# Optimization experiments

Hardware: AMD Instinct MI355X
Metric: run time of the kernel (lower is better)

The kernel has to match this reference:

```python
import math
import jax, jax.numpy as jnp
import numpy as np

DIM = 1024
N_HEADS = 16
N_KV_HEADS = 4
HEAD_DIM = 64
WINDOW = 512
EPS = 1e-6
B, S = 2, 2048

def _alibi_slopes(n_heads):
    def pow2(n):
        r = 2.0 ** (-8.0 / n)
        return np.array([r ** (i + 1) for i in range(n)], dtype=np.float32)
    if math.log2(n_heads).is_integer():
        return pow2(n_heads)
    m = 2 ** math.floor(math.log2(n_heads))
    return np.concatenate([pow2(m), pow2(2 * m)[::2][: n_heads - m]])

def _rmsnorm(x, w, eps=EPS):
    var = jnp.mean(x * x, axis=-1, keepdims=True)
    return x * jax.lax.rsqrt(var + eps) * w

def setup_inputs() -> dict:
    key = jax.random.key(0)
    ks = jax.random.split(key, 8)
    x = jax.random.normal(ks[0], (B, S, DIM), dtype=jnp.float32)
    wq = 0.02 * jax.random.normal(ks[1], (N_HEADS * HEAD_DIM, DIM), dtype=jnp.float32)
    wk = 0.02 * jax.random.normal(ks[2], (N_KV_HEADS * HEAD_DIM, DIM), dtype=jnp.float32)
    wv = 0.02 * jax.random.normal(ks[3], (N_KV_HEADS * HEAD_DIM, DIM), dtype=jnp.float32)
    wo = 0.02 * jax.random.normal(ks[4], (DIM, N_HEADS * HEAD_DIM), dtype=jnp.float32)
    q_norm_w = jnp.ones((N_HEADS * HEAD_DIM,), dtype=jnp.float32)
    k_norm_w = jnp.ones((N_KV_HEADS * HEAD_DIM,), dtype=jnp.float32)
    return {"x": x, "wq": wq, "wk": wk, "wv": wv, "wo": wo,
            "q_norm_w": q_norm_w, "k_norm_w": k_norm_w}

def reference(x, wq, wk, wv, wo, q_norm_w, k_norm_w):
    bsz, seqlen, _ = x.shape
    repeats = N_HEADS // N_KV_HEADS
    xq = _rmsnorm(x @ wq.T, q_norm_w)
    xk = _rmsnorm(x @ wk.T, k_norm_w)
    xv = x @ wv.T
    # [b, h, s, d]
    q = xq.reshape(bsz, seqlen, N_HEADS, HEAD_DIM).transpose(0, 2, 1, 3)
    k = xk.reshape(bsz, seqlen, N_KV_HEADS, HEAD_DIM).transpose(0, 2, 1, 3)
    v = xv.reshape(bsz, seqlen, N_KV_HEADS, HEAD_DIM).transpose(0, 2, 1, 3)
    k = jnp.repeat(k, repeats, axis=1)
    v = jnp.repeat(v, repeats, axis=1)
    pos = jnp.arange(seqlen)
    rel = pos[None, :] - pos[:, None]  # [s_q, s_k], key - query
    slopes = jnp.asarray(_alibi_slopes(N_HEADS))
    bias = slopes[:, None, None] * rel[None].astype(x.dtype)  # [h, s, s]
    masked = (rel > 0) | (rel < -WINDOW)  # causal + sliding window
    bias = jnp.where(masked[None], -jnp.inf, bias)
    scale = 1.0 / math.sqrt(HEAD_DIM)
    scores = jnp.einsum('bhqd,bhkd->bhqk', q, k) * scale + bias[None]
    probs = jax.nn.softmax(scores, axis=-1)
    y = jnp.einsum('bhqk,bhkd->bhqd', probs, v)
    y = y.transpose(0, 2, 1, 3).reshape(bsz, seqlen, N_HEADS * HEAD_DIM)
    return y @ wo.T
```

## Files before the change

kernel.cpp:

```cpp
#include <hip/hip_runtime.h>

typedef unsigned short u16;
typedef unsigned int u32;

typedef __bf16 bf16x8 __attribute__((ext_vector_type(8)));
typedef float f32x4 __attribute__((ext_vector_type(4)));

__device__ __forceinline__ u16 f2bf(float f) {
  u32 u = __builtin_bit_cast(u32, f);
  u32 r = (u + 0x7fffu + ((u >> 16) & 1u)) >> 16;
  return (u16)r;
}
__device__ __forceinline__ float bf2f(u16 v) {
  u32 u = (u32)v << 16;
  return __builtin_bit_cast(float, u);
}

__global__ __launch_bounds__(256)
void cvt_all_kernel(const float* __restrict__ x, const float* __restrict__ wq,
                    const float* __restrict__ wk, const float* __restrict__ wv,
                    const float* __restrict__ wo, u16* __restrict__ x_bf,
                    u16* __restrict__ wcat_bf, u16* __restrict__ wo_bf) {
  int t = blockIdx.x * 256 + threadIdx.x;
  const float* src;
  u16* dst;
  if (t < 1048576) {
    src = x; dst = x_bf;
  } else if (t < 1310720) {
    src = wq; dst = wcat_bf; t -= 1048576;
  } else if (t < 1376256) {
    src = wk; dst = wcat_bf + 1048576; t -= 1310720;
  } else if (t < 1441792) {
    src = wv; dst = wcat_bf + 1310720; t -= 1376256;
  } else {
    src = wo; dst = wo_bf; t -= 1441792;
  }
  const int i = t * 4;
  float4 v = *(const float4*)(src + i);
  uint2 p;
  p.x = (u32)f2bf(v.x) | ((u32)f2bf(v.y) << 16);
  p.y = (u32)f2bf(v.z) | ((u32)f2bf(v.w) << 16);
  *(uint2*)(dst + i) = p;
}

template <typename OutT>
__global__ __launch_bounds__(256)
void gemm_bt_kernel(const u16* __restrict__ A, const u16* __restrict__ B,
                    OutT* __restrict__ C, int M, int N, int K) {
  __shared__ u16 As[64 * 64];
  __shared__ u16 Bs[128 * 64];
  const int tid = threadIdx.x;
  const int lane = tid & 63;
  const int wave = tid >> 6;
  const int wm = (wave >> 1) * 32;
  const int wn = (wave & 1) * 64;
  const int l15 = lane & 15;
  const int quad = lane >> 4;
  const int sw = l15 & 7;
  const size_t bm = (size_t)blockIdx.y * 64;
  const size_t bn = (size_t)blockIdx.x * 128;

  f32x4 acc[2][4];
#pragma unroll
  for (int i = 0; i < 2; ++i)
#pragma unroll
    for (int j = 0; j < 4; ++j) acc[i][j] = f32x4{0.f, 0.f, 0.f, 0.f};

  const int ra0 = tid >> 3, ba0 = tid & 7;
  const int ra1 = (tid + 256) >> 3, ba1 = tid & 7;
  const u16* Ap0 = A + (bm + ra0) * (size_t)K + ba0 * 8;
  const u16* Ap1 = A + (bm + ra1) * (size_t)K + ba1 * 8;
  const u16* Bp0 = B + (bn + ra0) * (size_t)K + ba0 * 8;
  const u16* Bp1 = B + (bn + ra1) * (size_t)K + ba1 * 8;
  const u16* Bp2 = B + (bn + ra0 + 64) * (size_t)K + ba0 * 8;
  const u16* Bp3 = B + (bn + ra1 + 64) * (size_t)K + ba1 * 8;
  const int wa0 = ra0 * 64 + ((ba0 ^ (ra0 & 7)) * 8);
  const int wa1 = ra1 * 64 + ((ba1 ^ (ra1 & 7)) * 8);
  const int wb2 = (ra0 + 64) * 64 + ((ba0 ^ (ra0 & 7)) * 8);
  const int wb3 = (ra1 + 64) * 64 + ((ba1 ^ (ra1 & 7)) * 8);

  uint4 a0 = *(const uint4*)Ap0, a1 = *(const uint4*)Ap1;
  uint4 b0 = *(const uint4*)Bp0, b1 = *(const uint4*)Bp1;
  uint4 b2 = *(const uint4*)Bp2, b3 = *(const uint4*)Bp3;

  for (int k0 = 0; k0 < K; k0 += 64) {
    __syncthreads();
    *(uint4*)(&As[wa0]) = a0;
    *(uint4*)(&As[wa1]) = a1;
    *(uint4*)(&Bs[wa0]) = b0;
    *(uint4*)(&Bs[wa1]) = b1;
    *(uint4*)(&Bs[wb2]) = b2;
    *(uint4*)(&Bs[wb3]) = b3;
    __syncthreads();
    const int kn = (k0 + 64 < K) ? k0 + 64 : 0;
    a0 = *(const uint4*)(Ap0 + kn);
    a1 = *(const uint4*)(Ap1 + kn);
    b0 = *(const uint4*)(Bp0 + kn);
    b1 = *(const uint4*)(Bp1 + kn);
    b2 = *(const uint4*)(Bp2 + kn);
    b3 = *(const uint4*)(Bp3 + kn);
#pragma unroll
    for (int h = 0; h < 2; ++h) {
      const int cb = (quad + 4 * h);
      bf16x8 af[2], bfr[4];
#pragma unroll
      for (int i = 0; i < 2; ++i)
        af[i] = *(const bf16x8*)(&As[(wm + i * 16 + l15) * 64 + ((cb ^ sw) * 8)]);
#pragma unroll
      for (int j = 0; j < 4; ++j)
        bfr[j] = *(const bf16x8*)(&Bs[(wn + j * 16 + l15) * 64 + ((cb ^ sw) * 8)]);
#pragma unroll
      for (int i = 0; i < 2; ++i)
#pragma unroll
        for (int j = 0; j < 4; ++j)
          acc[i][j] = __builtin_amdgcn_mfma_f32_16x16x32_bf16(af[i], bfr[j], acc[i][j], 0, 0, 0);
    }
  }

  const int rq = quad * 4;
#pragma unroll
  for (int i = 0; i < 2; ++i) {
#pragma unroll
    for (int r = 0; r < 4; ++r) {
      OutT* crow = C + (bm + wm + i * 16 + rq + r) * (size_t)N + bn + wn + l15;
#pragma unroll
      for (int j = 0; j < 4; ++j) {
        if constexpr (sizeof(OutT) == 2)
          crow[j * 16] = f2bf(acc[i][j][r]);
        else
          crow[j * 16] = acc[i][j][r];
      }
    }
  }
}

__global__ __launch_bounds__(256)
void norm_vtrans_kernel(u16* __restrict__ qkv, const float* __restrict__ qw,
                        const float* __restrict__ kw, u16* __restrict__ vt) {
  __shared__ u16 shmem[64 * 72];
  const int bid = blockIdx.x;
  const int tid = threadIdx.x;
  if (bid < 4096) {
    float* red = (float*)shmem;
    u16* row = qkv + (size_t)bid * 1536;
    uint2 pk = *(const uint2*)(row + tid * 4);
    float v0 = bf2f((u16)pk.x), v1 = bf2f((u16)(pk.x >> 16));
    float v2 = bf2f((u16)pk.y), v3 = bf2f((u16)(pk.y >> 16));
    float ss = v0 * v0 + v1 * v1 + v2 * v2 + v3 * v3;
#pragma unroll
    for (int off = 32; off > 0; off >>= 1) ss += __shfl_down(ss, off);
    if ((tid & 63) == 0) red[tid >> 6] = ss;
    __syncthreads();
    float tot = red[0] + red[1] + red[2] + red[3];
    float rn = rsqrtf(tot * (1.0f / 1024.0f) + 1e-6f);
    float4 w = *(const float4*)(qw + tid * 4);
    uint2 po;
    po.x = (u32)f2bf(v0 * rn * w.x) | ((u32)f2bf(v1 * rn * w.y) << 16);
    po.y = (u32)f2bf(v2 * rn * w.z) | ((u32)f2bf(v3 * rn * w.w) << 16);
    *(uint2*)(row + tid * 4) = po;
    if (tid < 64) {
      uint2 kp = *(const uint2*)(row + 1024 + tid * 4);
      float k0 = bf2f((u16)kp.x), k1 = bf2f((u16)(kp.x >> 16));
      float k2 = bf2f((u16)kp.y), k3 = bf2f((u16)(kp.y >> 16));
      float sk = k0 * k0 + k1 * k1 + k2 * k2 + k3 * k3;
#pragma unroll
      for (int off = 32; off > 0; off >>= 1) sk += __shfl_down(sk, off);
      float tk = __shfl(sk, 0);
      float rk = rsqrtf(tk * (1.0f / 256.0f) + 1e-6f);
      float4 w2 = *(const float4*)(kw + tid * 4);
      uint2 ko;
      ko.x = (u32)f2bf(k0 * rk * w2.x) | ((u32)f2bf(k1 * rk * w2.y) << 16);
      ko.y = (u32)f2bf(k2 * rk * w2.z) | ((u32)f2bf(k3 * rk * w2.w) << 16);
      *(uint2*)(row + 1024 + tid * 4) = ko;
    }
  } else {
    const int e = bid - 4096;
    const int t0 = (e & 31) * 64, kvh = (e >> 5) & 3, b = e >> 7;
    u16(*tile)[72] = (u16(*)[72])shmem;
    const int r = tid >> 2, c16 = (tid & 3) * 16;
    const u16* src = qkv + (size_t)(b * 2048 + t0 + r) * 1536 + 1280 + kvh * 64 + c16;
    *(uint4*)&tile[r][c16] = *(const uint4*)src;
    *(uint4*)&tile[r][c16 + 8] = *(const uint4*)(src + 8);
    __syncthreads();
    const int d = tid >> 2, t16 = (tid & 3) * 16;
    u16 o[16];
#pragma unroll
    for (int j = 0; j < 16; ++j) o[j] = tile[t16 + j][d];
    u16* dst = vt + (size_t)((b * 4 + kvh) * 64 + d) * 2048 + t0 + t16;
    *(uint4*)dst = *(uint4*)&o[0];
    *(uint4*)(dst + 8) = *(uint4*)&o[8];
  }
}

__global__ __launch_bounds__(512)
void attn_kernel(const u16* __restrict__ qkvbf, const u16* __restrict__ vt,
                 u16* __restrict__ ybf) {
  __shared__ u16 Ks[64 * 72];
  __shared__ u16 Vts[64 * 72];
  __shared__ u16 Ps[128 * 72];
  const int qt = blockIdx.x, h = blockIdx.y, b = blockIdx.z;
  const int kvh = h >> 2, q0 = qt * 128;
  const int tid = threadIdx.x, lane = tid & 63, w = tid >> 6;
  const int l15 = lane & 15, quad = lane >> 4;

  const u16* qrow = qkvbf + (size_t)(b * 2048 + q0 + w * 16 + l15) * 1536 + h * 64 + quad * 8;
  const bf16x8 qf0 = *(const bf16x8*)qrow;
  const bf16x8 qf1 = *(const bf16x8*)(qrow + 32);

  const int sr = tid >> 3, sc = (tid & 7) * 8;
  const u16* kbase = qkvbf + (size_t)(b * 2048 + sr) * 1536 + 1024 + kvh * 64 + sc;
  const u16* vbase = vt + (size_t)((b * 4 + kvh) * 64 + sr) * 2048 + sc;

  f32x4 O[4];
#pragma unroll
  for (int jd = 0; jd < 4; ++jd) O[jd] = f32x4{0.f, 0.f, 0.f, 0.f};
  float m_i = -1e30f, l_i = 0.f;
  const float LOG2E = 1.44269504f;
  const float sc2 = 0.125f * LOG2E;
  const float slope2 = exp2f(-0.5f * (float)(h + 1)) * LOG2E;
  const int c_lo = (q0 >= 512) ? (q0 - 512) : 0;
  const int c_hi = q0 + 64;
  const int myq_lo = q0 + w * 16;
  const int myq_hi = myq_lo + 15;
  const int myq = myq_lo + l15;

  uint4 kr = *(const uint4*)(kbase + (size_t)c_lo * 1536);
  uint4 vr = *(const uint4*)(vbase + c_lo);

  for (int c = c_lo; c <= c_hi; c += 64) {
    __syncthreads();
    *(uint4*)&Ks[sr * 72 + sc] = kr;
    *(uint4*)&Vts[sr * 72 + sc] = vr;
    __syncthreads();
    {
      const int cn = (c + 64 <= c_hi) ? c + 64 : c_lo;
      kr = *(const uint4*)(kbase + (size_t)cn * 1536);
      vr = *(const uint4*)(vbase + cn);
    }

    if (c > myq_hi || c + 63 < myq_lo - 512) continue;

    f32x4 st[4];
#pragma unroll
    for (int i = 0; i < 4; ++i) {
      bf16x8 a0 = *(const bf16x8*)&Ks[(i * 16 + l15) * 72 + quad * 8];
      bf16x8 a1 = *(const bf16x8*)&Ks[(i * 16 + l15) * 72 + 32 + quad * 8];
      f32x4 z = f32x4{0.f, 0.f, 0.f, 0.f};
      z = __builtin_amdgcn_mfma_f32_16x16x32_bf16(a0, qf0, z, 0, 0, 0);
      st[i] = __builtin_amdgcn_mfma_f32_16x16x32_bf16(a1, qf1, z, 0, 0, 0);
    }

    float sv[4][4];
    float rm = -1e30f;
    const bool interior = (c + 63 <= myq_lo) && (c + 512 >= myq_hi);
    if (interior) {
#pragma unroll
      for (int i = 0; i < 4; ++i)
#pragma unroll
        for (int r = 0; r < 4; ++r) {
          const int key = c + i * 16 + quad * 4 + r;
          float val = st[i][r] * sc2 + slope2 * (float)(key - myq);
          sv[i][r] = val;
          rm = fmaxf(rm, val);
        }
    } else {
#pragma unroll
      for (int i = 0; i < 4; ++i)
#pragma unroll
        for (int r = 0; r < 4; ++r) {
          const int key = c + i * 16 + quad * 4 + r;
          const int rel = key - myq;
          float val = (rel > 0 || rel < -512) ? -1e30f
                                              : st[i][r] * sc2 + slope2 * (float)rel;
          sv[i][r] = val;
          rm = fmaxf(rm, val);
        }
    }
    rm = fmaxf(rm, __shfl_xor(rm, 16));
    rm = fmaxf(rm, __shfl_xor(rm, 32));
    const float mn = fmaxf(m_i, rm);
    const float alpha = exp2f(m_i - mn);
    float ls = 0.f;
#pragma unroll
    for (int i = 0; i < 4; ++i) {
      float p0 = exp2f(sv[i][0] - mn);
      float p1 = exp2f(sv[i][1] - mn);
      float p2 = exp2f(sv[i][2] - mn);
      float p3 = exp2f(sv[i][3] - mn);
      ls += (p0 + p1) + (p2 + p3);
      uint2 pw;
      pw.x = (u32)f2bf(p0) | ((u32)f2bf(p1) << 16);
      pw.y = (u32)f2bf(p2) | ((u32)f2bf(p3) << 16);
      *(uint2*)&Ps[(w * 16 + l15) * 72 + i * 16 + quad * 4] = pw;
    }
    ls += __shfl_xor(ls, 16);
    ls += __shfl_xor(ls, 32);
    l_i = l_i * alpha + ls;
    m_i = mn;

    float ar[4];
#pragma unroll
    for (int r = 0; r < 4; ++r) ar[r] = __shfl(alpha, quad * 4 + r);
#pragma unroll
    for (int jd = 0; jd < 4; ++jd)
#pragma unroll
      for (int r = 0; r < 4; ++r) O[jd][r] *= ar[r];

    bf16x8 pf0 = *(const bf16x8*)&Ps[(w * 16 + l15) * 72 + quad * 8];
    bf16x8 pf1 = *(const bf16x8*)&Ps[(w * 16 + l15) * 72 + 32 + quad * 8];
#pragma unroll
    for (int jd = 0; jd < 4; ++jd) {
      bf16x8 v0 = *(const bf16x8*)&Vts[(jd * 16 + l15) * 72 + quad * 8];
      bf16x8 v1 = *(const bf16x8*)&Vts[(jd * 16 + l15) * 72 + 32 + quad * 8];
      O[jd] = __builtin_amdgcn_mfma_f32_16x16x32_bf16(pf0, v0, O[jd], 0, 0, 0);
      O[jd] = __builtin_amdgcn_mfma_f32_16x16x32_bf16(pf1, v1, O[jd], 0, 0, 0);
    }
  }

  float lr[4];
#pragma unroll
  for (int r = 0; r < 4; ++r) lr[r] = __shfl(l_i, quad * 4 + r);
#pragma unroll
  for (int r = 0; r < 4; ++r) {
    const float inv = 1.0f / lr[r];
    u16* orow = ybf + (size_t)(b * 2048 + q0 + w * 16 + quad * 4 + r) * 1024 + h * 64 + l15;
#pragma unroll
    for (int jd = 0; jd < 4; ++jd) orow[jd * 16] = f2bf(O[jd][r] * inv);
  }
}

extern "C" void kernel_launch(void* const* d_in, const int* in_sizes, int n_in,
                              void* d_out, int out_size, void* d_ws, size_t ws_size,
                              hipStream_t stream) {
  const float* x = (const float*)d_in[0];
  const float* wq = (const float*)d_in[1];
  const float* wk = (const float*)d_in[2];
  const float* wv = (const float*)d_in[3];
  const float* wo = (const float*)d_in[4];
  const float* qnw = (const float*)d_in[5];
  const float* knw = (const float*)d_in[6];
  float* out = (float*)d_out;
  char* ws = (char*)d_ws;

  u16* x_bf = (u16*)(ws);
  u16* wcat_bf = (u16*)(ws + 8388608);
  u16* wo_bf = (u16*)(ws + 11534336);
  u16* qkv_bf = (u16*)(ws + 13631488);
  u16* vt_bf = (u16*)(ws + 26214400);
  u16* y_bf = (u16*)(ws + 28311552);

  cvt_all_kernel<<<6656, 256, 0, stream>>>(x, wq, wk, wv, wo, x_bf, wcat_bf, wo_bf);

  gemm_bt_kernel<u16><<<dim3(12, 64), 256, 0, stream>>>(x_bf, wcat_bf, qkv_bf, 4096, 1536, 1024);
  norm_vtrans_kernel<<<4352, 256, 0, stream>>>(qkv_bf, qnw, knw, vt_bf);
  attn_kernel<<<dim3(16, 16, 2), 512, 0, stream>>>(qkv_bf, vt_bf, y_bf);
  gemm_bt_kernel<float><<<dim3(8, 64), 256, 0, stream>>>(y_bf, wo_bf, out, 4096, 1024, 1024);
}
```

Before: 159.1 us.

## Double-buffer GEMM and attention tiles with direct global-to-LDS loads

Both the GEMM and the attention kernel now copy tiles from global memory straight into LDS with global_load_lds into double-buffered shared arrays. This removes the register staging and one barrier per iteration. The read-side XOR swizzle is kept by permuting the global source addresses instead. The attention kernel also raises wave priority around its MFMA sections. The change relies on the direct loads finishing before the single barrier, and the diff adds no explicit vmcnt wait for that, so there is a risk of reading a tile before it has landed.

```diff
diff --git a/kernel.cpp b/kernel.cpp
--- a/kernel.cpp
+++ b/kernel.cpp
@@ -14,6 +14,12 @@
 __device__ __forceinline__ float bf2f(u16 v) {
   u32 u = (u32)v << 16;
   return __builtin_bit_cast(float, u);
+}
+
+typedef const __attribute__((address_space(1))) u32 gbl_u32;
+typedef __attribute__((address_space(3))) u32 lds_u32;
+__device__ __forceinline__ void gload_lds16(const u16* g, u16* l) {
+  __builtin_amdgcn_global_load_lds((gbl_u32*)g, (lds_u32*)l, 16, 0, 0);
 }
 
 __global__ __launch_bounds__(256)
@@ -47,8 +53,8 @@
 __global__ __launch_bounds__(256)
 void gemm_bt_kernel(const u16* __restrict__ A, const u16* __restrict__ B,
                     OutT* __restrict__ C, int M, int N, int K) {
-  __shared__ u16 As[64 * 64];
-  __shared__ u16 Bs[128 * 64];
+  __shared__ u16 As[2][64 * 64];
+  __shared__ u16 Bs[2][128 * 64];
   const int tid = threadIdx.x;
   const int lane = tid & 63;
   const int wave = tid >> 6;
@@ -66,56 +72,51 @@
 #pragma unroll
     for (int j = 0; j < 4; ++j) acc[i][j] = f32x4{0.f, 0.f, 0.f, 0.f};
 
-  const int ra0 = tid >> 3, ba0 = tid & 7;
-  const int ra1 = (tid + 256) >> 3, ba1 = tid & 7;
-  const u16* Ap0 = A + (bm + ra0) * (size_t)K + ba0 * 8;
-  const u16* Ap1 = A + (bm + ra1) * (size_t)K + ba1 * 8;
-  const u16* Bp0 = B + (bn + ra0) * (size_t)K + ba0 * 8;
-  const u16* Bp1 = B + (bn + ra1) * (size_t)K + ba1 * 8;
-  const u16* Bp2 = B + (bn + ra0 + 64) * (size_t)K + ba0 * 8;
-  const u16* Bp3 = B + (bn + ra1 + 64) * (size_t)K + ba1 * 8;
-  const int wa0 = ra0 * 64 + ((ba0 ^ (ra0 & 7)) * 8);
-  const int wa1 = ra1 * 64 + ((ba1 ^ (ra1 & 7)) * 8);
-  const int wb2 = (ra0 + 64) * 64 + ((ba0 ^ (ra0 & 7)) * 8);
-  const int wb3 = (ra1 + 64) * 64 + ((ba1 ^ (ra1 & 7)) * 8);
-
-  uint4 a0 = *(const uint4*)Ap0, a1 = *(const uint4*)Ap1;
-  uint4 b0 = *(const uint4*)Bp0, b1 = *(const uint4*)Bp1;
-  uint4 b2 = *(const uint4*)Bp2, b3 = *(const uint4*)Bp3;
-
+  const int r0 = tid >> 3;
+  const int bswz = ((tid & 7) ^ (r0 & 7)) * 8;
+  const u16* gA0 = A + (bm + r0) * (size_t)K + bswz;
+  const u16* gA1 = A + (bm + r0 + 32) * (size_t)K + bswz;
+  const u16* gB0 = B + (bn + r0) * (size_t)K + bswz;
+  const u16* gB1 = B + (bn + r0 + 32) * (size_t)K + bswz;
+  const u16* gB2 = B + (bn + r0 + 64) * (size_t)K + bswz;
+  const u16* gB3 = B + (bn + r0 + 96) * (size_t)K + bswz;
+
+#define STAGE(bufi, kk)                                   \
+  do {                                                    \
+    gload_lds16(gA0 + (kk), &As[bufi][tid * 8]);          \
+    gload_lds16(gA1 + (kk), &As[bufi][2048 + tid * 8]);   \
+    gload_lds16(gB0 + (kk), &Bs[bufi][tid * 8]);          \
+    gload_lds16(gB1 + (kk), &Bs[bufi][2048 + tid * 8]);   \
+    gload_lds16(gB2 + (kk), &Bs[bufi][4096 + tid * 8]);   \
+    gload_lds16(gB3 + (kk), &Bs[bufi][6144 + tid * 8]);   \
+  } while (0)
+
+  STAGE(0, 0);
+  int buf = 0;
   for (int k0 = 0; k0 < K; k0 += 64) {
     __syncthreads();
-    *(uint4*)(&As[wa0]) = a0;
-    *(uint4*)(&As[wa1]) = a1;
-    *(uint4*)(&Bs[wa0]) = b0;
-    *(uint4*)(&Bs[wa1]) = b1;
-    *(uint4*)(&Bs[wb2]) = b2;
-    *(uint4*)(&Bs[wb3]) = b3;
-    __syncthreads();
-    const int kn = (k0 + 64 < K) ? k0 + 64 : 0;
-    a0 = *(const uint4*)(Ap0 + kn);
-    a1 = *(const uint4*)(Ap1 + kn);
-    b0 = *(const uint4*)(Bp0 + kn);
-    b1 = *(const uint4*)(Bp1 + kn);
-    b2 = *(const uint4*)(Bp2 + kn);
-    b3 = *(const uint4*)(Bp3 + kn);
+    if (k0 + 64 < K) STAGE(buf ^ 1, k0 + 64);
+    const u16* as = As[buf];
+    const u16* bs = Bs[buf];
 #pragma unroll
     for (int h = 0; h < 2; ++h) {
-      const int cb = (quad + 4 * h);
+      const int cb = quad + 4 * h;
       bf16x8 af[2], bfr[4];
 #pragma unroll
       for (int i = 0; i < 2; ++i)
-        af[i] = *(const bf16x8*)(&As[(wm + i * 16 + l15) * 64 + ((cb ^ sw) * 8)]);
+        af[i] = *(const bf16x8*)(&as[(wm + i * 16 + l15) * 64 + ((cb ^ sw) * 8)]);
 #pragma unroll
       for (int j = 0; j < 4; ++j)
-        bfr[j] = *(const bf16x8*)(&Bs[(wn + j * 16 + l15) * 64 + ((cb ^ sw) * 8)]);
+        bfr[j] = *(const bf16x8*)(&bs[(wn + j * 16 + l15) * 64 + ((cb ^ sw) * 8)]);
 #pragma unroll
       for (int i = 0; i < 2; ++i)
 #pragma unroll
         for (int j = 0; j < 4; ++j)
           acc[i][j] = __builtin_amdgcn_mfma_f32_16x16x32_bf16(af[i], bfr[j], acc[i][j], 0, 0, 0);
     }
-  }
+    buf ^= 1;
+  }
+#undef STAGE
 
   const int rq = quad * 4;
 #pragma unroll
@@ -195,21 +196,29 @@
 __global__ __launch_bounds__(512)
 void attn_kernel(const u16* __restrict__ qkvbf, const u16* __restrict__ vt,
                  u16* __restrict__ ybf) {
-  __shared__ u16 Ks[64 * 72];
-  __shared__ u16 Vts[64 * 72];
+  __shared__ u16 Ks[2][64 * 64];
+  __shared__ u16 Vts[2][64 * 64];
   __shared__ u16 Ps[128 * 72];
   const int qt = blockIdx.x, h = blockIdx.y, b = blockIdx.z;
   const int kvh = h >> 2, q0 = qt * 128;
   const int tid = threadIdx.x, lane = tid & 63, w = tid >> 6;
   const int l15 = lane & 15, quad = lane >> 4;
+  const int swl = l15 & 7;
 
   const u16* qrow = qkvbf + (size_t)(b * 2048 + q0 + w * 16 + l15) * 1536 + h * 64 + quad * 8;
   const bf16x8 qf0 = *(const bf16x8*)qrow;
   const bf16x8 qf1 = *(const bf16x8*)(qrow + 32);
 
-  const int sr = tid >> 3, sc = (tid & 7) * 8;
-  const u16* kbase = qkvbf + (size_t)(b * 2048 + sr) * 1536 + 1024 + kvh * 64 + sc;
-  const u16* vbase = vt + (size_t)((b * 4 + kvh) * 64 + sr) * 2048 + sc;
+  const int sr = tid >> 3;
+  const int bswz = ((tid & 7) ^ (sr & 7)) * 8;
+  const u16* kg = qkvbf + (size_t)(b * 2048 + sr) * 1536 + 1024 + kvh * 64 + bswz;
+  const u16* vg = vt + (size_t)((b * 4 + kvh) * 64 + sr) * 2048 + bswz;
+
+#define ASTAGE(bufi, cc)                                          \
+  do {                                                            \
+    gload_lds16(kg + (size_t)(cc) * 1536, &Ks[bufi][tid * 8]);    \
+    gload_lds16(vg + (cc), &Vts[bufi][tid * 8]);                  \
+  } while (0)
 
   f32x4 O[4];
 #pragma unroll
@@ -224,98 +233,99 @@
   const int myq_hi = myq_lo + 15;
   const int myq = myq_lo + l15;
 
-  uint4 kr = *(const uint4*)(kbase + (size_t)c_lo * 1536);
-  uint4 vr = *(const uint4*)(vbase + c_lo);
+  ASTAGE(0, c_lo);
+  int buf = 0;
 
   for (int c = c_lo; c <= c_hi; c += 64) {
     __syncthreads();
-    *(uint4*)&Ks[sr * 72 + sc] = kr;
-    *(uint4*)&Vts[sr * 72 + sc] = vr;
-    __syncthreads();
-    {
-      const int cn = (c + 64 <= c_hi) ? c + 64 : c_lo;
-      kr = *(const uint4*)(kbase + (size_t)cn * 1536);
-      vr = *(const uint4*)(vbase + cn);
+    if (c + 64 <= c_hi) ASTAGE(buf ^ 1, c + 64);
+
+    if (!(c > myq_hi || c + 63 < myq_lo - 512)) {
+      f32x4 st[4];
+      __builtin_amdgcn_s_setprio(1);
+#pragma unroll
+      for (int i = 0; i < 4; ++i) {
+        const int ro = (i * 16 + l15) * 64;
+        bf16x8 a0 = *(const bf16x8*)&Ks[buf][ro + ((quad ^ swl) * 8)];
+        bf16x8 a1 = *(const bf16x8*)&Ks[buf][ro + (((4 + quad) ^ swl) * 8)];
+        f32x4 z = f32x4{0.f, 0.f, 0.f, 0.f};
+        z = __builtin_amdgcn_mfma_f32_16x16x32_bf16(a0, qf0, z, 0, 0, 0);
+        st[i] = __builtin_amdgcn_mfma_f32_16x16x32_bf16(a1, qf1, st[i] = z, 0, 0, 0);
+      }
+      __builtin_amdgcn_s_setprio(0);
+
+      float sv[4][4];
+      float rm = -1e30f;
+      const bool interior = (c + 63 <= myq_lo) && (c + 512 >= myq_hi);
+      if (interior) {
+#pragma unroll
+        for (int i = 0; i < 4; ++i)
+#pragma unroll
+          for (int r = 0; r < 4; ++r) {
+            const int key = c + i * 16 + quad * 4 + r;
+            float val = st[i][r] * sc2 + slope2 * (float)(key - myq);
+            sv[i][r] = val;
+            rm = fmaxf(rm, val);
+          }
+      } else {
+#pragma unroll
+        for (int i = 0; i < 4; ++i)
+#pragma unroll
+          for (int r = 0; r < 4; ++r) {
+            const int key = c + i * 16 + quad * 4 + r;
+            const int rel = key - myq;
+            float val = (rel > 0 || rel < -512) ? -1e30f
+                                                : st[i][r] * sc2 + slope2 * (float)rel;
+            sv[i][r] = val;
+            rm = fmaxf(rm, val);
+          }
+      }
+      rm = fmaxf(rm, __shfl_xor(rm, 16));
+      rm = fmaxf(rm, __shfl_xor(rm, 32));
+      const float mn = fmaxf(m_i, rm);
+      const float alpha = exp2f(m_i - mn);
+      float ls = 0.f;
+#pragma unroll
+      for (int i = 0; i < 4; ++i) {
+        float p0 = exp2f(sv[i][0] - mn);
+        float p1 = exp2f(sv[i][1] - mn);
+        float p2 = exp2f(sv[i][2] - mn);
+        float p3 = exp2f(sv[i][3] - mn);
+        ls += (p0 + p1) + (p2 + p3);
+        uint2 pw;
+        pw.x = (u32)f2bf(p0) | ((u32)f2bf(p1) << 16);
+        pw.y = (u32)f2bf(p2) | ((u32)f2bf(p3) << 16);
+        *(uint2*)&Ps[(w * 16 + l15) * 72 + i * 16 + quad * 4] = pw;
+      }
+      ls += __shfl_xor(ls, 16);
+      ls += __shfl_xor(ls, 32);
+      l_i = l_i * alpha + ls;
+      m_i = mn;
+
+      float ar[4];
+#pragma unroll
+      for (int r = 0; r < 4; ++r) ar[r] = __shfl(alpha, quad * 4 + r);
+#pragma unroll
+      for (int jd = 0; jd < 4; ++jd)
+#pragma unroll
+        for (int r = 0; r < 4; ++r) O[jd][r] *= ar[r];
+
+      bf16x8 pf0 = *(const bf16x8*)&Ps[(w * 16 + l15) * 72 + quad * 8];
+      bf16x8 pf1 = *(const bf16x8*)&Ps[(w * 16 + l15) * 72 + 32 + quad * 8];
+      __builtin_amdgcn_s_setprio(1);
+#pragma unroll
+      for (int jd = 0; jd < 4; ++jd) {
+        const int ro = (jd * 16 + l15) * 64;
+        bf16x8 v0 = *(const bf16x8*)&Vts[buf][ro + ((quad ^ swl) * 8)];
+        bf16x8 v1 = *(const bf16x8*)&Vts[buf][ro + (((4 + quad) ^ swl) * 8)];
+        O[jd] = __builtin_amdgcn_mfma_f32_16x16x32_bf16(pf0, v0, O[jd], 0, 0, 0);
+        O[jd] = __builtin_amdgcn_mfma_f32_16x16x32_bf16(pf1, v1, O[jd], 0, 0, 0);
+      }
+      __builtin_amdgcn_s_setprio(0);
     }
-
-    if (c > myq_hi || c + 63 < myq_lo - 512) continue;
-
-    f32x4 st[4];
-#pragma unroll
-    for (int i = 0; i < 4; ++i) {
-      bf16x8 a0 = *(const bf16x8*)&Ks[(i * 16 + l15) * 72 + quad * 8];
-      bf16x8 a1 = *(const bf16x8*)&Ks[(i * 16 + l15) * 72 + 32 + quad * 8];
-      f32x4 z = f32x4{0.f, 0.f, 0.f, 0.f};
-      z = __builtin_amdgcn_mfma_f32_16x16x32_bf16(a0, qf0, z, 0, 0, 0);
-      st[i] = __builtin_amdgcn_mfma_f32_16x16x32_bf16(a1, qf1, z, 0, 0, 0);
-    }
-
-    float sv[4][4];
-    float rm = -1e30f;
-    const bool interior = (c + 63 <= myq_lo) && (c + 512 >= myq_hi);
-    if (interior) {
-#pragma unroll
-      for (int i = 0; i < 4; ++i)
-#pragma unroll
-        for (int r = 0; r < 4; ++r) {
-          const int key = c + i * 16 + quad * 4 + r;
-          float val = st[i][r] * sc2 + slope2 * (float)(key - myq);
-          sv[i][r] = val;
-          rm = fmaxf(rm, val);
-        }
-    } else {
-#pragma unroll
-      for (int i = 0; i < 4; ++i)
-#pragma unroll
-        for (int r = 0; r < 4; ++r) {
-          const int key = c + i * 16 + quad * 4 + r;
-          const int rel = key - myq;
-          float val = (rel > 0 || rel < -512) ? -1e30f
-                                              : st[i][r] * sc2 + slope2 * (float)rel;
-          sv[i][r] = val;
-          rm = fmaxf(rm, val);
-        }
-    }
-    rm = fmaxf(rm, __shfl_xor(rm, 16));
-    rm = fmaxf(rm, __shfl_xor(rm, 32));
-    const float mn = fmaxf(m_i, rm);
-    const float alpha = exp2f(m_i - mn);
-    float ls = 0.f;
-#pragma unroll
-    for (int i = 0; i < 4; ++i) {
-      float p0 = exp2f(sv[i][0] - mn);
-      float p1 = exp2f(sv[i][1] - mn);
-      float p2 = exp2f(sv[i][2] - mn);
-      float p3 = exp2f(sv[i][3] - mn);
-      ls += (p0 + p1) + (p2 + p3);
-      uint2 pw;
-      pw.x = (u32)f2bf(p0) | ((u32)f2bf(p1) << 16);
-      pw.y = (u32)f2bf(p2) | ((u32)f2bf(p3) << 16);
-      *(uint2*)&Ps[(w * 16 + l15) * 72 + i * 16 + quad * 4] = pw;
-    }
-    ls += __shfl_xor(ls, 16);
-    ls += __shfl_xor(ls, 32);
-    l_i = l_i * alpha + ls;
-    m_i = mn;
-
-    float ar[4];
-#pragma unroll
-    for (int r = 0; r < 4; ++r) ar[r] = __shfl(alpha, quad * 4 + r);
-#pragma unroll
-    for (int jd = 0; jd < 4; ++jd)
-#pragma unroll
-      for (int r = 0; r < 4; ++r) O[jd][r] *= ar[r];
-
-    bf16x8 pf0 = *(const bf16x8*)&Ps[(w * 16 + l15) * 72 + quad * 8];
-    bf16x8 pf1 = *(const bf16x8*)&Ps[(w * 16 + l15) * 72 + 32 + quad * 8];
-#pragma unroll
-    for (int jd = 0; jd < 4; ++jd) {
-      bf16x8 v0 = *(const bf16x8*)&Vts[(jd * 16 + l15) * 72 + quad * 8];
-      bf16x8 v1 = *(const bf16x8*)&Vts[(jd * 16 + l15) * 72 + 32 + quad * 8];
-      O[jd] = __builtin_amdgcn_mfma_f32_16x16x32_bf16(pf0, v0, O[jd], 0, 0, 0);
-      O[jd] = __builtin_amdgcn_mfma_f32_16x16x32_bf16(pf1, v1, O[jd], 0, 0, 0);
-    }
-  }
+    buf ^= 1;
+  }
+#undef ASTAGE
 
   float lr[4];
 #pragma unroll
```

Measured after the change: 158.0 us. Within noise of the previous version (-0.7%).
